# Performance work log

Measured on AMD Instinct MI355X. Metric: run time of the kernel, lower is better.

The kernel has to match this reference:

```python
import jax, jax.numpy as jnp
import numpy as np


def setup_inputs() -> dict:
    key = jax.random.key(0)
    k1, k2 = jax.random.split(key)
    query = jax.random.normal(k1, (32, 1, 1024), dtype=jnp.float32)
    keys = jax.random.normal(k2, (32, 4096, 1024), dtype=jnp.float32)
    return {"query": query, "keys": keys}


def reference(query, keys):
    # scores: (B, S) = keys (B,S,H) @ query (B,H,1), no 1/sqrt(d) scaling (faithful to source)
    scores = jnp.einsum("bsh,bh->bs", keys, query[:, 0, :])
    attention_weights = jax.nn.softmax(scores, axis=1)  # (B, S)
    # context: weighted sum of keys (module uses keys as values)
    context_vector = jnp.einsum("bs,bsh->bh", attention_weights, keys)  # (B, H)
    return (context_vector, attention_weights)
```

## Files before the change

### kernel.cpp

```cpp
#include <hip/hip_runtime.h>

#define BATCH 32
#define S 4096
#define H 1024
#define H4 (H / 4)
#define NCHUNK 32
#define KPC (S / NCHUNK)
#define BLOCK 256
#define NWAVE (BLOCK / 64)
#define KPW (KPC / NWAVE)

typedef float vfloat4 __attribute__((ext_vector_type(4)));

static __device__ __forceinline__ vfloat4 nt_load(const vfloat4* p) {
  return __builtin_nontemporal_load(p);
}

__global__ __launch_bounds__(BLOCK) void attn_pass1(
    const float* __restrict__ query, const float* __restrict__ keys,
    float* __restrict__ scores,
    float* __restrict__ po,
    float* __restrict__ pm,
    float* __restrict__ pl)
{
  const int chunk = blockIdx.x;
  const int b     = blockIdx.y;
  const int lane  = threadIdx.x & 63;
  const int wave  = threadIdx.x >> 6;

  const vfloat4* q4 = (const vfloat4*)(query + (size_t)b * H);
  const vfloat4 q0 = q4[lane], q1 = q4[lane + 64], q2 = q4[lane + 128], q3 = q4[lane + 192];

  const int s0 = chunk * KPC + wave * KPW;
  const vfloat4* kp = (const vfloat4*)(keys + ((size_t)b * S + s0) * (size_t)H);

  vfloat4 k0 = nt_load(kp + lane), k1 = nt_load(kp + lane + 64),
          k2 = nt_load(kp + lane + 128), k3 = nt_load(kp + lane + 192);

  float m = -3.0e38f, l = 0.0f;
  vfloat4 o0 = {0,0,0,0}, o1 = {0,0,0,0}, o2 = {0,0,0,0}, o3 = {0,0,0,0};

  for (int i = 0; i < KPW; ++i) {
    const vfloat4* kn = (i + 1 < KPW) ? (kp + H4) : kp;
    const vfloat4 n0 = nt_load(kn + lane),       n1 = nt_load(kn + lane + 64),
                  n2 = nt_load(kn + lane + 128), n3 = nt_load(kn + lane + 192);

    float d = k0.x*q0.x + k0.y*q0.y + k0.z*q0.z + k0.w*q0.w
            + k1.x*q1.x + k1.y*q1.y + k1.z*q1.z + k1.w*q1.w
            + k2.x*q2.x + k2.y*q2.y + k2.z*q2.z + k2.w*q2.w
            + k3.x*q3.x + k3.y*q3.y + k3.z*q3.z + k3.w*q3.w;
    #pragma unroll
    for (int off = 1; off < 64; off <<= 1) d += __shfl_xor(d, off);

    if (lane == 0) scores[(size_t)b * S + (s0 + i)] = d;

    const float mn = fmaxf(m, d);
    const float sc = __expf(m - mn);
    const float p  = __expf(d - mn);
    l = l * sc + p;
    o0 = o0*sc + p*k0;
    o1 = o1*sc + p*k1;
    o2 = o2*sc + p*k2;
    o3 = o3*sc + p*k3;
    m = mn;
    k0 = n0; k1 = n1; k2 = n2; k3 = n3;
    kp = kn;
  }

  __shared__ float lds_o[NWAVE][H];
  __shared__ float lds_m[NWAVE], lds_l[NWAVE];
  vfloat4* lo = (vfloat4*)lds_o[wave];
  lo[lane] = o0; lo[lane + 64] = o1; lo[lane + 128] = o2; lo[lane + 192] = o3;
  if (lane == 0) { lds_m[wave] = m; lds_l[wave] = l; }
  __syncthreads();

  const int t = threadIdx.x;
  const float bm = fmaxf(fmaxf(lds_m[0], lds_m[1]), fmaxf(lds_m[2], lds_m[3]));
  float bl = 0.0f;
  vfloat4 acc = {0,0,0,0};
  #pragma unroll
  for (int w = 0; w < NWAVE; ++w) {
    const float scw = __expf(lds_m[w] - bm);
    bl += lds_l[w] * scw;
    const vfloat4 ow = ((const vfloat4*)lds_o[w])[t];
    acc += ow * scw;
  }
  ((vfloat4*)po)[((size_t)b * NCHUNK + chunk) * H4 + t] = acc;
  if (t == 0) { pm[b * NCHUNK + chunk] = bm; pl[b * NCHUNK + chunk] = bl; }
}

__global__ __launch_bounds__(256) void attn_pass2(
    const float* __restrict__ po, const float* __restrict__ pm, const float* __restrict__ pl,
    float* __restrict__ ctx, float* __restrict__ wts)
{
  const int b = blockIdx.x;
  const int t = threadIdx.x;
  __shared__ float s_scale[NCHUNK];
  __shared__ float s_m, s_invl;
  if (t == 0) {
    float m = -3.0e38f;
    for (int j = 0; j < NCHUNK; ++j) m = fmaxf(m, pm[b * NCHUNK + j]);
    float l = 0.0f;
    for (int j = 0; j < NCHUNK; ++j) {
      const float sc = __expf(pm[b * NCHUNK + j] - m);
      s_scale[j] = sc;
      l += pl[b * NCHUNK + j] * sc;
    }
    s_m = m; s_invl = 1.0f / l;
  }
  __syncthreads();
  const float m = s_m, invl = s_invl;

  vfloat4 acc = {0,0,0,0};
  for (int j = 0; j < NCHUNK; ++j) {
    const vfloat4 ow = ((const vfloat4*)po)[((size_t)b * NCHUNK + j) * H4 + t];
    acc += ow * s_scale[j];
  }
  acc *= invl;
  ((vfloat4*)ctx)[(size_t)b * H4 + t] = acc;

  for (int s = t; s < S; s += 256) {
    const float sc = wts[(size_t)b * S + s];
    wts[(size_t)b * S + s] = __expf(sc - m) * invl;
  }
}

extern "C" void kernel_launch(void* const* d_in, const int* in_sizes, int n_in,
                              void* d_out, int out_size, void* d_ws, size_t ws_size,
                              hipStream_t stream) {
  const float* query = (const float*)d_in[0];
  const float* keys  = (const float*)d_in[1];

  float* ctx = (float*)d_out;
  float* wts = (float*)d_out + BATCH * H;

  float* po = (float*)d_ws;
  float* pm = po + (size_t)BATCH * NCHUNK * H;
  float* pl = pm + BATCH * NCHUNK;

  attn_pass1<<<dim3(NCHUNK, BATCH), BLOCK, 0, stream>>>(query, keys, wts, po, pm, pl);
  attn_pass2<<<BATCH, 256, 0, stream>>>(po, pm, pl, ctx, wts);
}
```

Measured before the change: 663.9 us.

## Stage key tiles into LDS via double-buffered global_load_lds with fewer chunks

Replaces the per-wave register prefetch of one key row with block-wide asynchronous global-to-LDS loads of 8-row tiles, double-buffered so the next tile streams in while the current one is consumed. The chunk count is halved, so each block covers more rows and fewer partials reach the second pass. The aim is more bytes in flight and less load-latency stall on a purely bandwidth-bound stream. The trade-offs are 64KB of LDS per block, which limits resident blocks per CU, and a barrier per tile.

```diff
diff --git a/kernel.cpp b/kernel.cpp
--- a/kernel.cpp
+++ b/kernel.cpp
@@ -1,20 +1,19 @@
 #include <hip/hip_runtime.h>
+#include <stdint.h>
 
 #define BATCH 32
 #define S 4096
 #define H 1024
 #define H4 (H / 4)
-#define NCHUNK 32
+#define NCHUNK 16
 #define KPC (S / NCHUNK)
 #define BLOCK 256
 #define NWAVE (BLOCK / 64)
-#define KPW (KPC / NWAVE)
+#define TROWS 8
+#define NTILES (KPC / TROWS)
+#define RPW (TROWS / NWAVE)
 
 typedef float vfloat4 __attribute__((ext_vector_type(4)));
-
-static __device__ __forceinline__ vfloat4 nt_load(const vfloat4* p) {
-  return __builtin_nontemporal_load(p);
-}
 
 __global__ __launch_bounds__(BLOCK) void attn_pass1(
     const float* __restrict__ query, const float* __restrict__ keys,
@@ -28,53 +27,78 @@
   const int lane  = threadIdx.x & 63;
   const int wave  = threadIdx.x >> 6;
 
+  __shared__ __align__(16) float buf[2][TROWS][H];
+  __shared__ float lds_m[NWAVE], lds_l[NWAVE];
+
   const vfloat4* q4 = (const vfloat4*)(query + (size_t)b * H);
   const vfloat4 q0 = q4[lane], q1 = q4[lane + 64], q2 = q4[lane + 128], q3 = q4[lane + 192];
 
-  const int s0 = chunk * KPC + wave * KPW;
-  const vfloat4* kp = (const vfloat4*)(keys + ((size_t)b * S + s0) * (size_t)H);
+  const float* kb = keys + ((size_t)b * S + (size_t)chunk * KPC) * (size_t)H;
 
-  vfloat4 k0 = nt_load(kp + lane), k1 = nt_load(kp + lane + 64),
-          k2 = nt_load(kp + lane + 128), k3 = nt_load(kp + lane + 192);
+  auto stage = [&](int t, int pb) {
+    #pragma unroll
+    for (int r = 0; r < RPW; ++r) {
+      const int row = wave * RPW + r;
+      const float* g = kb + (size_t)(t * TROWS + row) * H + lane * 4;
+      #pragma unroll
+      for (int qo = 0; qo < 4; ++qo) {
+        __builtin_amdgcn_global_load_lds(
+            (const __attribute__((address_space(1))) uint32_t*)(g + qo * 256),
+            (__attribute__((address_space(3))) uint32_t*)(&buf[pb][row][qo * 256]),
+            16, 0, 0);
+      }
+    }
+  };
 
   float m = -3.0e38f, l = 0.0f;
   vfloat4 o0 = {0,0,0,0}, o1 = {0,0,0,0}, o2 = {0,0,0,0}, o3 = {0,0,0,0};
 
-  for (int i = 0; i < KPW; ++i) {
-    const vfloat4* kn = (i + 1 < KPW) ? (kp + H4) : kp;
-    const vfloat4 n0 = nt_load(kn + lane),       n1 = nt_load(kn + lane + 64),
-                  n2 = nt_load(kn + lane + 128), n3 = nt_load(kn + lane + 192);
+  stage(0, 0);
+  __syncthreads();
 
-    float d = k0.x*q0.x + k0.y*q0.y + k0.z*q0.z + k0.w*q0.w
-            + k1.x*q1.x + k1.y*q1.y + k1.z*q1.z + k1.w*q1.w
-            + k2.x*q2.x + k2.y*q2.y + k2.z*q2.z + k2.w*q2.w
-            + k3.x*q3.x + k3.y*q3.y + k3.z*q3.z + k3.w*q3.w;
+  int pb = 0;
+  for (int t = 0; t < NTILES; ++t) {
+    if (t + 1 < NTILES) stage(t + 1, pb ^ 1);
+
     #pragma unroll
-    for (int off = 1; off < 64; off <<= 1) d += __shfl_xor(d, off);
+    for (int r = 0; r < RPW; ++r) {
+      const int row = wave * RPW + r;
+      const vfloat4* lrow = (const vfloat4*)&buf[pb][row][0];
+      const vfloat4 k0 = lrow[lane],       k1 = lrow[lane + 64],
+                    k2 = lrow[lane + 128], k3 = lrow[lane + 192];
 
-    if (lane == 0) scores[(size_t)b * S + (s0 + i)] = d;
+      float d0 = k0.x*q0.x + k0.y*q0.y + k0.z*q0.z + k0.w*q0.w;
+      float d1 = k1.x*q1.x + k1.y*q1.y + k1.z*q1.z + k1.w*q1.w;
+      float d2 = k2.x*q2.x + k2.y*q2.y + k2.z*q2.z + k2.w*q2.w;
+      float d3 = k3.x*q3.x + k3.y*q3.y + k3.z*q3.z + k3.w*q3.w;
+      float d  = (d0 + d1) + (d2 + d3);
+      #pragma unroll
+      for (int off = 1; off < 64; off <<= 1) d += __shfl_xor(d, off);
 
-    const float mn = fmaxf(m, d);
-    const float sc = __expf(m - mn);
-    const float p  = __expf(d - mn);
-    l = l * sc + p;
-    o0 = o0*sc + p*k0;
-    o1 = o1*sc + p*k1;
-    o2 = o2*sc + p*k2;
-    o3 = o3*sc + p*k3;
-    m = mn;
-    k0 = n0; k1 = n1; k2 = n2; k3 = n3;
-    kp = kn;
+      if (lane == 0) scores[(size_t)b * S + chunk * KPC + t * TROWS + row] = d;
+
+      const float mn = fmaxf(m, d);
+      const float sc = __expf(m - mn);
+      const float p  = __expf(d - mn);
+      l  = l * sc + p;
+      o0 = o0*sc + p*k0;
+      o1 = o1*sc + p*k1;
+      o2 = o2*sc + p*k2;
+      o3 = o3*sc + p*k3;
+      m = mn;
+    }
+
+    __syncthreads();
+    pb ^= 1;
   }
 
-  __shared__ float lds_o[NWAVE][H];
-  __shared__ float lds_m[NWAVE], lds_l[NWAVE];
-  vfloat4* lo = (vfloat4*)lds_o[wave];
+  float* red = &buf[0][0][0];
+  vfloat4* lo = (vfloat4*)(red + wave * H);
   lo[lane] = o0; lo[lane + 64] = o1; lo[lane + 128] = o2; lo[lane + 192] = o3;
   if (lane == 0) { lds_m[wave] = m; lds_l[wave] = l; }
   __syncthreads();
 
-  const int t = threadIdx.x;
+  const int tid = threadIdx.x;
   const float bm = fmaxf(fmaxf(lds_m[0], lds_m[1]), fmaxf(lds_m[2], lds_m[3]));
   float bl = 0.0f;
   vfloat4 acc = {0,0,0,0};
@@ -82,11 +106,11 @@
   for (int w = 0; w < NWAVE; ++w) {
     const float scw = __expf(lds_m[w] - bm);
     bl += lds_l[w] * scw;
-    const vfloat4 ow = ((const vfloat4*)lds_o[w])[t];
+    const vfloat4 ow = ((const vfloat4*)(red + w * H))[tid];
     acc += ow * scw;
   }
-  ((vfloat4*)po)[((size_t)b * NCHUNK + chunk) * H4 + t] = acc;
-  if (t == 0) { pm[b * NCHUNK + chunk] = bm; pl[b * NCHUNK + chunk] = bl; }
+  ((vfloat4*)po)[((size_t)b * NCHUNK + chunk) * H4 + tid] = acc;
+  if (tid == 0) { pm[b * NCHUNK + chunk] = bm; pl[b * NCHUNK + chunk] = bl; }
 }
 
 __global__ __launch_bounds__(256) void attn_pass2(
```

After: 684.3 us. +3.1%, slower.
